# Performance work log

Measured on AMD Instinct MI355X. Metric: run time of the kernel, lower is better.

## Reference

```python
import jax, jax.numpy as jnp
import numpy as np

V, E, HID, NLAYERS, NL, B, T = 21128, 512, 512, 2, 9, 64, 512
H = HID // 2  # per-direction hidden


def setup_inputs() -> dict:
    key = jax.random.key(0)
    ks = jax.random.split(key, 12)
    n = lambda k, sh, sc=0.05: (jax.random.normal(k, sh, dtype=jnp.float32) * sc)
    return {
        "input_ids": jax.random.randint(ks[0], (B, T), 0, V),
        "labels": jax.random.randint(ks[1], (B, T), 0, NL),
        "emb": n(ks[2], (V, E), 0.02),
        # stacked LSTM params: [layer, direction, ...]; layer0 input = E == HID
        "w_ih": n(ks[3], (NLAYERS, 2, 4 * H, HID)),
        "w_hh": n(ks[4], (NLAYERS, 2, 4 * H, H)),
        "b_ih": n(ks[5], (NLAYERS, 2, 4 * H)),
        "b_hh": n(ks[6], (NLAYERS, 2, 4 * H)),
        "cls_w": n(ks[7], (NL, HID)),
        "cls_b": n(ks[8], (NL,)),
        "start_trans": jax.random.uniform(ks[9], (NL,), jnp.float32, -0.1, 0.1),
        "end_trans": jax.random.uniform(ks[10], (NL,), jnp.float32, -0.1, 0.1),
        "trans": jax.random.uniform(ks[11], (NL, NL), jnp.float32, -0.1, 0.1),
    }


def _lstm_dir(x, wi, wh, bi, bh, reverse):
    # x: [B,T,I] -> h: [B,T,H]; torch gate order i,f,g,o
    xp = jnp.einsum('bti,gi->btg', x, wi) + bi + bh  # [B,T,4H]
    if reverse:
        xp = xp[:, ::-1]
    h0 = jnp.zeros((x.shape[0], wh.shape[1]), x.dtype)

    def step(carry, xt):
        h, c = carry
        g = xt + h @ wh.T
        i, f, gg, o = jnp.split(g, 4, axis=-1)
        c = jax.nn.sigmoid(f) * c + jax.nn.sigmoid(i) * jnp.tanh(gg)
        h = jax.nn.sigmoid(o) * jnp.tanh(c)
        return (h, c), h

    _, hs = jax.lax.scan(step, (h0, h0), xp.swapaxes(0, 1))
    hs = hs.swapaxes(0, 1)
    return hs[:, ::-1] if reverse else hs


def _crf_neg_llh(logits, labels, start_trans, end_trans, trans):
    # torchcrf forward, full mask, reduction='sum'; returns -sum(log-likelihood)
    em0 = logits[:, 0]  # [B,NL]
    alpha0 = start_trans[None, :] + em0
    num0 = start_trans[labels[:, 0]] + jnp.take_along_axis(em0, labels[:, 0:1], 1)[:, 0]

    def step(carry, xt):
        alpha, num, prev = carry
        em, tag = xt  # [B,NL], [B]
        alpha = jax.nn.logsumexp(alpha[:, :, None] + trans[None] + em[:, None, :], axis=1)
        num = num + trans[prev, tag] + jnp.take_along_axis(em, tag[:, None], 1)[:, 0]
        return (alpha, num, tag), None

    xs = (logits[:, 1:].swapaxes(0, 1), labels[:, 1:].swapaxes(0, 1))
    (alpha, num, last), _ = jax.lax.scan(step, (alpha0, num0, labels[:, 0]), xs)
    denom = jax.nn.logsumexp(alpha + end_trans[None, :], axis=1)
    num = num + end_trans[last]
    return -jnp.sum(num - denom)


def reference(input_ids, labels, emb, w_ih, w_hh, b_ih, b_hh, cls_w, cls_b,
              start_trans, end_trans, trans):
    x = emb[input_ids]  # [B,T,E]
    for l in range(NLAYERS):
        fwd = _lstm_dir(x, w_ih[l, 0], w_hh[l, 0], b_ih[l, 0], b_hh[l, 0], False)
        bwd = _lstm_dir(x, w_ih[l, 1], w_hh[l, 1], b_ih[l, 1], b_hh[l, 1], True)
        x = jnp.concatenate([fwd, bwd], axis=-1)  # [B,T,HID]
    logits = jnp.einsum('bth,lh->btl', x, cls_w) + cls_b  # [B,T,NL]
    return _crf_neg_llh(logits, labels, start_trans, end_trans, trans)
```

## Files before the change

### kernel.cpp

```cpp
#include <hip/hip_runtime.h>

#define B_   64
#define T_   512
#define HID_ 512
#define H_   256
#define G4   1024
#define N2   2048
#define M_   (B_*T_)
#define NL_  9

typedef short short8 __attribute__((ext_vector_type(8)));
typedef float f32x4 __attribute__((ext_vector_type(4)));
typedef _Float16 f16x2 __attribute__((ext_vector_type(2)));

__device__ inline float bf2f(unsigned short u) {
  unsigned int x = ((unsigned int)u) << 16;
  return __builtin_bit_cast(float, x);
}
__device__ inline unsigned short f2bf(float f) {
  unsigned int u = __builtin_bit_cast(unsigned int, f);
  return (unsigned short)((u + 0x7fffu + ((u >> 16) & 1u)) >> 16);
}
__device__ inline unsigned short f2h(float f) {
  _Float16 h = (_Float16)f;
  return __builtin_bit_cast(unsigned short, h);
}
__device__ inline float fdot2(unsigned int w, unsigned int h, float acc) {
#if __has_builtin(__builtin_amdgcn_fdot2)
  return __builtin_amdgcn_fdot2(__builtin_bit_cast(f16x2, w),
                                __builtin_bit_cast(f16x2, h), acc, false);
#else
  f16x2 a = __builtin_bit_cast(f16x2, w), b = __builtin_bit_cast(f16x2, h);
  return acc + (float)a[0]*(float)b[0] + (float)a[1]*(float)b[1];
#endif
}
__device__ inline float sigm(float x)     { return 1.f / (1.f + __expf(-x)); }
__device__ inline float tanhfast(float x) { return 1.f - 2.f / (__expf(2.f*x) + 1.f); }

__device__ inline float xhalf_sum(float x) {
#if __has_builtin(__builtin_amdgcn_permlane32_swap)
  typedef unsigned int u32x2 __attribute__((ext_vector_type(2)));
  u32x2 r = __builtin_amdgcn_permlane32_swap(
      __builtin_bit_cast(unsigned int, x), __builtin_bit_cast(unsigned int, x),
      false, false);
  return x + __builtin_bit_cast(float, r[1]);
#else
  return x + __shfl_xor(x, 32, 64);
#endif
}

__device__ inline void gload16(const unsigned short* g, unsigned short* l) {
  __builtin_amdgcn_global_load_lds(
      (const __attribute__((address_space(1))) void*)g,
      (__attribute__((address_space(3))) void*)l, 16, 0, 0);
}

__global__ void k_cast_bf16(const float* __restrict__ src, unsigned short* __restrict__ dst, int n) {
  int i = blockIdx.x*256 + threadIdx.x;
  if (i < n) dst[i] = f2bf(src[i]);
}

__global__ void k_pack_whh(const float* __restrict__ whh, unsigned int* __restrict__ wr,
                           unsigned int* __restrict__ wl) {
  int idx = blockIdx.x*256 + threadIdx.x;
  int q   = idx & 3;
  int t   = (idx >> 2) & 511;
  int i4  = (idx >> 11) & 63;
  int ld  = idx >> 17;
  int lane = t & 63, wave = t >> 6;
  int u  = wave*32 + (lane & 31);
  int kh = lane >> 5;
  int g, k0;
  if (i4 < 48) { g = i4/12; int j = i4%12; k0 = kh*128 + 8*j + 2*q; }
  else         { int m = i4-48; g = m>>2; int jl = m&3; k0 = kh*128 + 96 + 8*jl + 2*q; }
  int c = g*256 + u;
  const float* src = whh + ((size_t)ld*1024 + c)*256 + k0;
  unsigned int pack = (unsigned int)f2h(src[0]) | ((unsigned int)f2h(src[1]) << 16);
  if (i4 < 48) wr[(((size_t)ld*48 + i4)*512 + t)*4 + q];
  if (i4 < 48) wr[(((size_t)ld*48 + i4)*512 + t)*4 + q] = pack;
  else         wl[(((size_t)ld*16 + (i4-48))*512 + t)*4 + q] = pack;
}

__global__ void k_bias_sum(const float* __restrict__ bi, const float* __restrict__ bh,
                           float* __restrict__ bs) {
  int i = blockIdx.x*256 + threadIdx.x;
  if (i < 4096) bs[i] = bi[i] + bh[i];
}

__global__ void k_cls_pad(const float* __restrict__ w, unsigned short* __restrict__ dst) {
  int i = blockIdx.x*256 + threadIdx.x;
  if (i < 16*512) {
    int n = i >> 9, k = i & 511;
    dst[i] = (n < NL_) ? f2bf(w[n*512 + k]) : (unsigned short)0;
  }
}

__global__ void k_embed(const int* __restrict__ ids, const float* __restrict__ emb,
                        unsigned short* __restrict__ x0) {
  int idx = blockIdx.x*256 + threadIdx.x;
  int m  = idx >> 7;
  int e4 = (idx & 127) << 2;
  int id = ids[m];
  float4 v = *(const float4*)(emb + (size_t)id*HID_ + e4);
  unsigned short* dst = x0 + (size_t)m*HID_ + e4;
  dst[0]=f2bf(v.x); dst[1]=f2bf(v.y); dst[2]=f2bf(v.z); dst[3]=f2bf(v.w);
}

__global__ __launch_bounds__(256) void k_gemm_inproj(const unsigned short* __restrict__ A,
    const unsigned short* __restrict__ Bt, const float* __restrict__ bias,
    unsigned short* __restrict__ C) {
  __shared__ unsigned short As[4096];
  __shared__ unsigned short Bs[4096];
  int tid  = threadIdx.x;
  int lane = tid & 63, w = tid >> 6;
  int wm = w >> 1, wn = w & 1;
  int n0 = blockIdx.x * 128;
  int m0 = blockIdx.y * 128;

  int c0 = tid, c1 = 256 + tid;
  int ar0 = c0 & 127, ak0 = c0 >> 7;
  int ar1 = c1 & 127, ak1 = c1 >> 7;
  const unsigned short* gA0 = A  + (size_t)(m0 + ar0)*512 + ak0*8;
  const unsigned short* gA1 = A  + (size_t)(m0 + ar1)*512 + ak1*8;
  const unsigned short* gB0 = Bt + (size_t)(n0 + ar0)*512 + ak0*8;
  const unsigned short* gB1 = Bt + (size_t)(n0 + ar1)*512 + ak1*8;
  unsigned short* lA0 = As + (size_t)c0*8;
  unsigned short* lA1 = As + (size_t)c1*8;
  unsigned short* lB0 = Bs + (size_t)c0*8;
  unsigned short* lB1 = Bs + (size_t)c1*8;

  int r = lane & 15, kg = lane >> 4;
  const short8* Af = (const short8*)As + (size_t)kg*128 + wm*64 + r;
  const short8* Bf = (const short8*)Bs + (size_t)kg*128 + wn*64 + r;

  f32x4 acc[4][4];
  #pragma unroll
  for (int mi = 0; mi < 4; mi++)
    #pragma unroll
    for (int ni = 0; ni < 4; ni++)
      acc[mi][ni] = (f32x4){0,0,0,0};

  #pragma unroll 1
  for (int kt = 0; kt < 16; kt++) {
    gload16(gA0, lA0); gload16(gA1, lA1);
    gload16(gB0, lB0); gload16(gB1, lB1);
    gA0 += 32; gA1 += 32; gB0 += 32; gB1 += 32;
    __syncthreads();
    short8 av[4], bv[4];
    #pragma unroll
    for (int i = 0; i < 4; i++) { av[i] = Af[i*16]; bv[i] = Bf[i*16]; }
    #pragma unroll
    for (int mi = 0; mi < 4; mi++)
      #pragma unroll
      for (int ni = 0; ni < 4; ni++)
        acc[mi][ni] = __builtin_amdgcn_mfma_f32_16x16x32_bf16(av[mi], bv[ni], acc[mi][ni], 0, 0, 0);
    __syncthreads();
  }

  int rbase = m0 + wm*64 + (lane >> 4)*4;
  int cbase = n0 + wn*64 + (lane & 15);
  #pragma unroll
  for (int ni = 0; ni < 4; ni++) {
    float bb = bias[cbase + ni*16];
    #pragma unroll
    for (int mi = 0; mi < 4; mi++)
      #pragma unroll
      for (int rr = 0; rr < 4; rr++)
        C[(size_t)(rbase + mi*16 + rr)*N2 + cbase + ni*16] = f2bf(acc[mi][ni][rr] + bb);
  }
}

__global__ __launch_bounds__(256) void k_cls(const unsigned short* __restrict__ X,
    const unsigned short* __restrict__ Wb, const float* __restrict__ cb,
    float* __restrict__ out) {
  int lane = threadIdx.x & 63, wave = threadIdx.x >> 6;
  int m0 = blockIdx.x*64 + wave*16;
  int r = lane & 15, kg = lane >> 4;
  const short8* Ap = (const short8*)(X  + (size_t)(m0 + r)*512 + kg*8);
  const short8* Bp = (const short8*)(Wb + (size_t)r*512 + kg*8);
  f32x4 acc = {0,0,0,0};
  #pragma unroll
  for (int kb = 0; kb < 16; kb++)
    acc = __builtin_amdgcn_mfma_f32_16x16x32_bf16(Ap[kb*4], Bp[kb*4], acc, 0, 0, 0);
  int row0 = m0 + (lane >> 4)*4, col = lane & 15;
  if (col < NL_) {
    float bb = cb[col];
    #pragma unroll
    for (int rr = 0; rr < 4; rr++)
      out[(size_t)(row0+rr)*NL_ + col] = acc[rr] + bb;
  }
}

#define DOT4(ACC, W0, W1, W2, W3, HH) do { \
  ACC = fdot2(W0, (HH).x, ACC); ACC = fdot2(W1, (HH).y, ACC); \
  ACC = fdot2(W2, (HH).z, ACC); ACC = fdot2(W3, (HH).w, ACC); } while(0)

__global__ __launch_bounds__(512, 2) void k_rec(const unsigned short* __restrict__ xp,
    const uint4* __restrict__ wr, const uint4* __restrict__ wl,
    unsigned short* __restrict__ xout, int layer) {
  extern __shared__ char smem[];
  unsigned int* hA = (unsigned int*)(smem + 131072);
  unsigned int* hB = hA + 128;
  int t = threadIdx.x;
  int lane = t & 63, wave = t >> 6;
  int u  = wave*32 + (lane & 31);
  int kh = lane >> 5;
  bool lo = (lane < 32);
  int b = blockIdx.x >> 1, d = blockIdx.x & 1;
  int ld = layer*2 + d;

  char* wlb = smem + (((unsigned)(t*16)) ^ (((unsigned)t & 0x38u) << 1));
  {
    const uint4* src = wl + (size_t)ld*16*512 + t;
    #pragma unroll
    for (int m = 0; m < 16; m++)
      *(uint4*)(wlb + m*8192) = src[(size_t)m*512];
  }
  uint4 wq[48];
  {
    const uint4* src = wr + (size_t)ld*48*512 + t;
    #pragma unroll
    for (int i = 0; i < 48; i++) wq[i] = src[(size_t)i*512];
  }
  if (t < 128) hA[t] = 0u;
  float cst = 0.f;
  const unsigned short* xbase = xp + (size_t)b*T_*N2 + (size_t)d*G4 + u;
  unsigned short* obase = xout + (size_t)b*T_*HID_ + d*H_ + u;
  __syncthreads();

  int tt = d ? (T_-1) : 0;
  float nx0=0.f, nx1=0.f, nx2=0.f, nx3=0.f;
  if (lo) {
    const unsigned short* xr = xbase + (size_t)tt*N2;
    nx0 = bf2f(xr[0]); nx1 = bf2f(xr[256]); nx2 = bf2f(xr[512]); nx3 = bf2f(xr[768]);
  }
  #pragma unroll 1
  for (int step = 0; step < T_; step++) {
    const uint4* hs = (const uint4*)((step & 1) ? hB : hA) + kh*16;
    float a0 = lo ? nx0 : 0.f, a1 = lo ? nx1 : 0.f;
    float a2 = lo ? nx2 : 0.f, a3 = lo ? nx3 : 0.f;
    int ttn = d ? (T_-2-step) : (step+1);
    if (lo && step < T_-1) {
      const unsigned short* xr = xbase + (size_t)ttn*N2;
      nx0 = bf2f(xr[0]); nx1 = bf2f(xr[256]); nx2 = bf2f(xr[512]); nx3 = bf2f(xr[768]);
    }
    #pragma unroll
    for (int j = 0; j < 12; j++) {
      uint4 hh = hs[j];
      DOT4(a0, wq[j].x,    wq[j].y,    wq[j].z,    wq[j].w,    hh);
      DOT4(a1, wq[12+j].x, wq[12+j].y, wq[12+j].z, wq[12+j].w, hh);
      DOT4(a2, wq[24+j].x, wq[24+j].y, wq[24+j].z, wq[24+j].w, hh);
      DOT4(a3, wq[36+j].x, wq[36+j].y, wq[36+j].z, wq[36+j].w, hh);
    }
    #pragma unroll
    for (int jl = 0; jl < 4; jl++) {
      uint4 hh = hs[12 + jl];
      uint4 q0 = *(const uint4*)(wlb + (0*4+jl)*8192);
      uint4 q1 = *(const uint4*)(wlb + (1*4+jl)*8192);
      uint4 q2 = *(const uint4*)(wlb + (2*4+jl)*8192);
      uint4 q3 = *(const uint4*)(wlb + (3*4+jl)*8192);
      DOT4(a0, q0.x, q0.y, q0.z, q0.w, hh);
      DOT4(a1, q1.x, q1.y, q1.z, q1.w, hh);
      DOT4(a2, q2.x, q2.y, q2.z, q2.w, hh);
      DOT4(a3, q3.x, q3.y, q3.z, q3.w, hh);
    }
    a0 = xhalf_sum(a0); a1 = xhalf_sum(a1);
    a2 = xhalf_sum(a2); a3 = xhalf_sum(a3);
    if (lo) {
      float gi = sigm(a0);
      float gf = sigm(a1);
      float gg = tanhfast(a2);
      float go = sigm(a3);
      cst = gf*cst + gi*gg;
      float h = go * tanhfast(cst);
      _Float16* hn = (_Float16*)((step & 1) ? hA : hB);
      hn[u] = (_Float16)h;
      obase[(size_t)tt*HID_] = f2bf(h);
    }
    __syncthreads();
    tt = ttn;
  }
}

__global__ void k_zero(float* out) { if (threadIdx.x == 0) out[0] = 0.f; }

__global__ void k_crf(const float* __restrict__ logits, const int* __restrict__ labels,
                      const float* __restrict__ st, const float* __restrict__ et,
                      const float* __restrict__ tr, float* __restrict__ out) {
  int b = blockIdx.x, lane = threadIdx.x;
  bool act = lane < NL_;
  const float* lb = logits + (size_t)b*T_*NL_;
  float trc[9];
  #pragma unroll
  for (int i = 0; i < 9; i++) trc[i] = act ? tr[i*9 + lane] : 0.f;
  float em = act ? lb[lane] : -1e30f;
  float alpha = act ? (st[lane] + em) : -1e30f;
  int prev = labels[b*T_];
  float num = __shfl(alpha, prev);
  for (int ttt = 1; ttt < T_; ttt++) {
    em = act ? lb[ttt*NL_ + lane] : -1e30f;
    float vv[9]; float mx = -1e30f;
    #pragma unroll
    for (int i = 0; i < 9; i++) { vv[i] = __shfl(alpha, i) + trc[i]; mx = fmaxf(mx, vv[i]); }
    float s = 0.f;
    #pragma unroll
    for (int i = 0; i < 9; i++) s += __expf(vv[i] - mx);
    alpha = act ? (mx + __logf(s) + em) : -1e30f;
    int tag = labels[b*T_ + ttt];
    float emtag = __shfl(em, tag);
    if (lane == 0) num += tr[prev*9 + tag] + emtag;
    prev = tag;
  }
  float fa = act ? (alpha + et[lane]) : -1e30f;
  float mx = -1e30f;
  #pragma unroll
  for (int i = 0; i < 9; i++) mx = fmaxf(mx, __shfl(fa, i));
  float s = 0.f;
  #pragma unroll
  for (int i = 0; i < 9; i++) s += __expf(__shfl(fa, i) - mx);
  float denom = mx + __logf(s);
  if (lane == 0) {
    num += et[prev];
    atomicAdd(out, denom - num);
  }
}

extern "C" void kernel_launch(void* const* d_in, const int* in_sizes, int n_in,
                              void* d_out, int out_size, void* d_ws, size_t ws_size,
                              hipStream_t stream) {
  const int*   ids    = (const int*)d_in[0];
  const int*   labels = (const int*)d_in[1];
  const float* emb    = (const float*)d_in[2];
  const float* w_ih   = (const float*)d_in[3];
  const float* w_hh   = (const float*)d_in[4];
  const float* b_ih   = (const float*)d_in[5];
  const float* b_hh   = (const float*)d_in[6];
  const float* cls_w  = (const float*)d_in[7];
  const float* cls_b  = (const float*)d_in[8];
  const float* st     = (const float*)d_in[9];
  const float* et     = (const float*)d_in[10];
  const float* tr     = (const float*)d_in[11];
  float* out = (float*)d_out;

  char* ws = (char*)d_ws;
  unsigned short* xp    = (unsigned short*)(ws);
  unsigned short* x0    = (unsigned short*)(ws + 134217728);
  unsigned short* x1    = (unsigned short*)(ws + 167772160);
  unsigned short* wbi   = (unsigned short*)(ws + 201326592);
  unsigned int*   wreg  = (unsigned int*)  (ws + 205520896);
  unsigned int*   wldsg = (unsigned int*)  (ws + 207093760);
  float*          bsum  = (float*)         (ws + 207618048);
  unsigned short* clswb = (unsigned short*)(ws + 207634432);
  float*          logit = (float*)         (ws + 207650816);

  const int REC_SMEM = 131072 + 1024;
  hipFuncSetAttribute((const void*)k_rec, hipFuncAttributeMaxDynamicSharedMemorySize, REC_SMEM);

  k_cast_bf16<<<8192, 256, 0, stream>>>(w_ih, wbi, 2*N2*512);
  k_pack_whh <<<2048, 256, 0, stream>>>(w_hh, wreg, wldsg);
  k_bias_sum <<<16,   256, 0, stream>>>(b_ih, b_hh, bsum);
  k_cls_pad  <<<32,   256, 0, stream>>>(cls_w, clswb);
  k_embed    <<<16384,256, 0, stream>>>(ids, emb, x0);

  dim3 ggrid(16, 256);
  k_gemm_inproj<<<ggrid, 256, 0, stream>>>(x0, wbi, bsum, xp);
  k_rec<<<128, 512, REC_SMEM, stream>>>(xp, (const uint4*)wreg, (const uint4*)wldsg, x1, 0);
  k_gemm_inproj<<<ggrid, 256, 0, stream>>>(x1, wbi + (size_t)N2*512, bsum + 2048, xp);
  k_rec<<<128, 512, REC_SMEM, stream>>>(xp, (const uint4*)wreg, (const uint4*)wldsg, x0, 1);
  k_cls<<<512, 256, 0, stream>>>(x0, clswb, cls_b, logit);
  k_zero<<<1, 64, 0, stream>>>(out);
  k_crf<<<64, 64, 0, stream>>>(logit, labels, st, et, tr, out);
}
```

Measured before the change: 2.528 ms.

## Process two batch sequences per recurrent block to reuse register-resident weights

The recurrent LSTM kernel now handles two batch rows (b0 and b0+32) per block instead of one. Each weight value loaded from registers or LDS is applied to both hidden states, so the grid halves from 128 to 64 blocks. The goal is to amortise weight reads and the per-step barrier across twice the work. The cost is more live registers (a second set of accumulators and inputs), which risks spilling given 48 uint4 weight registers, and using only half as many CUs; per-step latency also grows.

Result: slower. 4.118 ms (+62.9%).

```diff
diff --git a/kernel.cpp b/kernel.cpp
--- a/kernel.cpp
+++ b/kernel.cpp
@@ -76,7 +76,6 @@
   int c = g*256 + u;
   const float* src = whh + ((size_t)ld*1024 + c)*256 + k0;
   unsigned int pack = (unsigned int)f2h(src[0]) | ((unsigned int)f2h(src[1]) << 16);
-  if (i4 < 48) wr[(((size_t)ld*48 + i4)*512 + t)*4 + q];
   if (i4 < 48) wr[(((size_t)ld*48 + i4)*512 + t)*4 + q] = pack;
   else         wl[(((size_t)ld*16 + (i4-48))*512 + t)*4 + q] = pack;
 }
@@ -199,14 +198,17 @@
     const uint4* __restrict__ wr, const uint4* __restrict__ wl,
     unsigned short* __restrict__ xout, int layer) {
   extern __shared__ char smem[];
-  unsigned int* hA = (unsigned int*)(smem + 131072);
-  unsigned int* hB = hA + 128;
+  unsigned int* hA0 = (unsigned int*)(smem + 131072);
+  unsigned int* hA1 = hA0 + 128;
+  unsigned int* hB0 = hA1 + 128;
+  unsigned int* hB1 = hB0 + 128;
   int t = threadIdx.x;
   int lane = t & 63, wave = t >> 6;
   int u  = wave*32 + (lane & 31);
   int kh = lane >> 5;
   bool lo = (lane < 32);
-  int b = blockIdx.x >> 1, d = blockIdx.x & 1;
+  int d  = blockIdx.x & 1;
+  int b0 = blockIdx.x >> 1;
   int ld = layer*2 + d;
 
   char* wlb = smem + (((unsigned)(t*16)) ^ (((unsigned)t & 0x38u) << 1));
@@ -222,60 +224,85 @@
     #pragma unroll
     for (int i = 0; i < 48; i++) wq[i] = src[(size_t)i*512];
   }
-  if (t < 128) hA[t] = 0u;
-  float cst = 0.f;
-  const unsigned short* xbase = xp + (size_t)b*T_*N2 + (size_t)d*G4 + u;
-  unsigned short* obase = xout + (size_t)b*T_*HID_ + d*H_ + u;
+  if (t < 128) { hA0[t] = 0u; hB0[t] = 0u; }
+  float cstA = 0.f, cstB = 0.f;
+  const unsigned short* xbA = xp + (size_t)b0*T_*N2        + (size_t)d*G4 + u;
+  const unsigned short* xbB = xp + (size_t)(b0+32)*T_*N2   + (size_t)d*G4 + u;
+  unsigned short* obA = xout + (size_t)b0*T_*HID_      + d*H_ + u;
+  unsigned short* obB = xout + (size_t)(b0+32)*T_*HID_ + d*H_ + u;
   __syncthreads();
 
   int tt = d ? (T_-1) : 0;
-  float nx0=0.f, nx1=0.f, nx2=0.f, nx3=0.f;
+  float nA0=0.f, nA1=0.f, nA2=0.f, nA3=0.f;
+  float nB0=0.f, nB1=0.f, nB2=0.f, nB3=0.f;
   if (lo) {
-    const unsigned short* xr = xbase + (size_t)tt*N2;
-    nx0 = bf2f(xr[0]); nx1 = bf2f(xr[256]); nx2 = bf2f(xr[512]); nx3 = bf2f(xr[768]);
+    const unsigned short* ra = xbA + (size_t)tt*N2;
+    const unsigned short* rb = xbB + (size_t)tt*N2;
+    nA0 = bf2f(ra[0]); nA1 = bf2f(ra[256]); nA2 = bf2f(ra[512]); nA3 = bf2f(ra[768]);
+    nB0 = bf2f(rb[0]); nB1 = bf2f(rb[256]); nB2 = bf2f(rb[512]); nB3 = bf2f(rb[768]);
   }
   #pragma unroll 1
   for (int step = 0; step < T_; step++) {
-    const uint4* hs = (const uint4*)((step & 1) ? hB : hA) + kh*16;
-    float a0 = lo ? nx0 : 0.f, a1 = lo ? nx1 : 0.f;
-    float a2 = lo ? nx2 : 0.f, a3 = lo ? nx3 : 0.f;
+    const uint4* hsA = (const uint4*)((step & 1) ? hA1 : hA0) + kh*16;
+    const uint4* hsB = (const uint4*)((step & 1) ? hB1 : hB0) + kh*16;
+    float aA0 = lo ? nA0 : 0.f, aA1 = lo ? nA1 : 0.f;
+    float aA2 = lo ? nA2 : 0.f, aA3 = lo ? nA3 : 0.f;
+    float aB0 = lo ? nB0 : 0.f, aB1 = lo ? nB1 : 0.f;
+    float aB2 = lo ? nB2 : 0.f, aB3 = lo ? nB3 : 0.f;
     int ttn = d ? (T_-2-step) : (step+1);
     if (lo && step < T_-1) {
-      const unsigned short* xr = xbase + (size_t)ttn*N2;
-      nx0 = bf2f(xr[0]); nx1 = bf2f(xr[256]); nx2 = bf2f(xr[512]); nx3 = bf2f(xr[768]);
+      const unsigned short* ra = xbA + (size_t)ttn*N2;
+      const unsigned short* rb = xbB + (size_t)ttn*N2;
+      nA0 = bf2f(ra[0]); nA1 = bf2f(ra[256]); nA2 = bf2f(ra[512]); nA3 = bf2f(ra[768]);
+      nB0 = bf2f(rb[0]); nB1 = bf2f(rb[256]); nB2 = bf2f(rb[512]); nB3 = bf2f(rb[768]);
     }
     #pragma unroll
     for (int j = 0; j < 12; j++) {
-      uint4 hh = hs[j];
-      DOT4(a0, wq[j].x,    wq[j].y,    wq[j].z,    wq[j].w,    hh);
-      DOT4(a1, wq[12+j].x, wq[12+j].y, wq[12+j].z, wq[12+j].w, hh);
-      DOT4(a2, wq[24+j].x, wq[24+j].y, wq[24+j].z, wq[24+j].w, hh);
-      DOT4(a3, wq[36+j].x, wq[36+j].y, wq[36+j].z, wq[36+j].w, hh);
+      uint4 ha = hsA[j], hb = hsB[j];
+      DOT4(aA0, wq[j].x,    wq[j].y,    wq[j].z,    wq[j].w,    ha);
+      DOT4(aB0, wq[j].x,    wq[j].y,    wq[j].z,    wq[j].w,    hb);
+      DOT4(aA1, wq[12+j].x, wq[12+j].y, wq[12+j].z, wq[12+j].w, ha);
+      DOT4(aB1, wq[12+j].x, wq[12+j].y, wq[12+j].z, wq[12+j].w, hb);
+      DOT4(aA2, wq[24+j].x, wq[24+j].y, wq[24+j].z, wq[24+j].w, ha);
+      DOT4(aB2, wq[24+j].x, wq[24+j].y, wq[24+j].z, wq[24+j].w, hb);
+      DOT4(aA3, wq[36+j].x, wq[36+j].y, wq[36+j].z, wq[36+j].w, ha);
+      DOT4(aB3, wq[36+j].x, wq[36+j].y, wq[36+j].z, wq[36+j].w, hb);
     }
     #pragma unroll
     for (int jl = 0; jl < 4; jl++) {
-      uint4 hh = hs[12 + jl];
+      uint4 ha = hsA[12 + jl], hb = hsB[12 + jl];
       uint4 q0 = *(const uint4*)(wlb + (0*4+jl)*8192);
       uint4 q1 = *(const uint4*)(wlb + (1*4+jl)*8192);
       uint4 q2 = *(const uint4*)(wlb + (2*4+jl)*8192);
       uint4 q3 = *(const uint4*)(wlb + (3*4+jl)*8192);
-      DOT4(a0, q0.x, q0.y, q0.z, q0.w, hh);
-      DOT4(a1, q1.x, q1.y, q1.z, q1.w, hh);
-      DOT4(a2, q2.x, q2.y, q2.z, q2.w, hh);
-      DOT4(a3, q3.x, q3.y, q3.z, q3.w, hh);
+      DOT4(aA0, q0.x, q0.y, q0.z, q0.w, ha);
+      DOT4(aB0, q0.x, q0.y, q0.z, q0.w, hb);
+      DOT4(aA1, q1.x, q1.y, q1.z, q1.w, ha);
+      DOT4(aB1, q1.x, q1.y, q1.z, q1.w, hb);
+      DOT4(aA2, q2.x, q2.y, q2.z, q2.w, ha);
+      DOT4(aB2, q2.x, q2.y, q2.z, q2.w, hb);
+      DOT4(aA3, q3.x, q3.y, q3.z, q3.w, ha);
+      DOT4(aB3, q3.x, q3.y, q3.z, q3.w, hb);
     }
-    a0 = xhalf_sum(a0); a1 = xhalf_sum(a1);
-    a2 = xhalf_sum(a2); a3 = xhalf_sum(a3);
+    aA0 = xhalf_sum(aA0); aA1 = xhalf_sum(aA1);
+    aA2 = xhalf_sum(aA2); aA3 = xhalf_sum(aA3);
+    aB0 = xhalf_sum(aB0); aB1 = xhalf_sum(aB1);
+    aB2 = xhalf_sum(aB2); aB3 = xhalf_sum(aB3);
     if (lo) {
-      float gi = sigm(a0);
-      float gf = sigm(a1);
-      float gg = tanhfast(a2);
-      float go = sigm(a3);
-      cst = gf*cst + gi*gg;
-      float h = go * tanhfast(cst);
-      _Float16* hn = (_Float16*)((step & 1) ? hA : hB);
-      hn[u] = (_Float16)h;
-      obase[(size_t)tt*HID_] = f2bf(h);
+      float giA = sigm(aA0), gfA = sigm(aA1);
+      float ggA = tanhfast(aA2), goA = sigm(aA3);
+      cstA = gfA*cstA + giA*ggA;
+      float hA = goA * tanhfast(cstA);
+      float giB = sigm(aB0), gfB = sigm(aB1);
+      float ggB = tanhfast(aB2), goB = sigm(aB3);
+      cstB = gfB*cstB + giB*ggB;
+      float hB = goB * tanhfast(cstB);
+      _Float16* hnA = (_Float16*)((step & 1) ? hA0 : hA1);
+      _Float16* hnB = (_Float16*)((step & 1) ? hB0 : hB1);
+      hnA[u] = (_Float16)hA;
+      hnB[u] = (_Float16)hB;
+      obA[(size_t)tt*HID_] = f2bf(hA);
+      obB[(size_t)tt*HID_] = f2bf(hB);
     }
     __syncthreads();
     tt = ttn;
@@ -353,7 +380,7 @@
   unsigned short* clswb = (unsigned short*)(ws + 207634432);
   float*          logit = (float*)         (ws + 207650816);
 
-  const int REC_SMEM = 131072 + 1024;
+  const int REC_SMEM = 131072 + 2048;
   hipFuncSetAttribute((const void*)k_rec, hipFuncAttributeMaxDynamicSharedMemorySize, REC_SMEM);
 
   k_cast_bf16<<<8192, 256, 0, stream>>>(w_ih, wbi, 2*N2*512);
@@ -364,9 +391,9 @@
 
   dim3 ggrid(16, 256);
   k_gemm_inproj<<<ggrid, 256, 0, stream>>>(x0, wbi, bsum, xp);
-  k_rec<<<128, 512, REC_SMEM, stream>>>(xp, (const uint4*)wreg, (const uint4*)wldsg, x1, 0);
+  k_rec<<<64, 512, REC_SMEM, stream>>>(xp, (const uint4*)wreg, (const uint4*)wldsg, x1, 0);
   k_gemm_inproj<<<ggrid, 256, 0, stream>>>(x1, wbi + (size_t)N2*512, bsum + 2048, xp);
-  k_rec<<<128, 512, REC_SMEM, stream>>>(xp, (const uint4*)wreg, (const uint4*)wldsg, x0, 1);
+  k_rec<<<64, 512, REC_SMEM, stream>>>(xp, (const uint4*)wreg, (const uint4*)wldsg, x0, 1);
   k_cls<<<512, 256, 0, stream>>>(x0, clswb, cls_b, logit);
   k_zero<<<1, 64, 0, stream>>>(out);
   k_crf<<<64, 64, 0, stream>>>(logit, labels, st, et, tr, out);
```
